# Performance work log

Hardware: AMD Instinct MI355X
Metric: run time of the kernel (lower is better)

The kernel has to match this reference:

```python
import jax, jax.numpy as jnp
import numpy as np

N_WIRES = 8


def setup_inputs() -> dict:
    key = jax.random.key(0)
    k1, k2, k3 = jax.random.split(key, 3)
    B, S, E = 8, 1024, 64
    x = jax.random.normal(k1, (B, S, E), jnp.float32)
    theta = jax.random.normal(k2, (N_WIRES,), jnp.float32) * 0.1  # trainable RX angles (shared QLayer across heads)
    V_CAT = 16
    combine_w = jax.random.normal(k3, (E, V_CAT), jnp.float32) / jnp.sqrt(jnp.float32(V_CAT))
    combine_b = jnp.zeros((E,), jnp.float32)
    return {"x": x, "theta": theta, "combine_w": combine_w, "combine_b": combine_b}


def _cnot(state, c, t):
    # state: [N] + [2]*N_WIRES ; wire w lives on axis w+1
    ca, ta = c + 1, t + 1
    s0 = jax.lax.index_in_dim(state, 0, axis=ca, keepdims=False)
    s1 = jax.lax.index_in_dim(state, 1, axis=ca, keepdims=False)
    ta2 = ta - 1 if ta > ca else ta  # control axis was removed
    s1 = jnp.flip(s1, axis=ta2)      # flip target bit where control == 1
    return jnp.stack([s0, s1], axis=ca)


def _qlayer(angles, theta):
    # angles: [N, 8]. RX(x) then trainable RX(theta) on same wire == RX(x+theta).
    half = 0.5 * (angles + theta)
    amp0 = jnp.cos(half).astype(jnp.complex64)          # <0|RX|0>
    amp1 = (-1j) * jnp.sin(half).astype(jnp.complex64)  # <1|RX|0>
    N = angles.shape[0]
    # product state over 8 wires -> [N, 256]
    state = jnp.ones((N, 1), jnp.complex64)
    for w in range(N_WIRES):
        per = jnp.stack([amp0[:, w], amp1[:, w]], axis=-1)  # [N, 2]
        state = (state[:, :, None] * per[:, None, :]).reshape(N, -1)
    state = state.reshape((N,) + (2,) * N_WIRES)
    # CNOT chain 0->1, ..., 6->7, then ring closure 7->0
    for w in range(N_WIRES - 1):
        state = _cnot(state, w, w + 1)
    state = _cnot(state, N_WIRES - 1, 0)
    probs = state.real ** 2 + state.imag ** 2
    exps = []
    for w in range(N_WIRES):
        axes = tuple(ax for ax in range(1, N_WIRES + 1) if ax != w + 1)
        marg = probs.sum(axis=axes)  # [N, 2]
        exps.append(marg[:, 0] - marg[:, 1])  # <Z_w>
    return jnp.stack(exps, axis=-1)  # [N, 8]


def reference(x, theta, combine_w, combine_b):
    B, S, E = x.shape
    d_k = E // N_WIRES  # == 8 (encoder needs exactly 8 angles)
    heads = x.reshape(B, S, N_WIRES, d_k).transpose(0, 2, 1, 3)  # [B, H, S, 8]
    meas = _qlayer(heads.reshape(-1, d_k), theta).reshape(B, N_WIRES, S, N_WIRES)
    # torch.chunk(3, -1) on size 8 -> splits of 3, 3, 2
    q, k, v = meas[..., :3], meas[..., 3:6], meas[..., 6:]
    scores = jnp.einsum('bhsd,bhtd->bhst', q, k) / jnp.sqrt(jnp.float32(E))
    attn = jax.nn.softmax(scores, axis=-1)
    out = jnp.einsum('bhst,bhtd->bhsd', attn, v)          # [B, H, S, 2]
    out = out.transpose(0, 2, 1, 3).reshape(B, S, -1)     # [B, S, 16]
    return out @ combine_w.T + combine_b
```

## Files before the change

kernel.cpp:

```cpp
#include <hip/hip_runtime.h>
#include <hip/hip_fp16.h>

#define NB 8
#define NS 1024
#define NH 8

typedef float f2 __attribute__((ext_vector_type(2)));

#if __has_builtin(__builtin_amdgcn_exp2f)
#define EXP2F(x) __builtin_amdgcn_exp2f(x)
#else
#define EXP2F(x) exp2f(x)
#endif


__global__ __launch_bounds__(256, 2) void attn_fused(
        const float* __restrict__ x, const float* __restrict__ theta,
        float* __restrict__ att) {
    __shared__ float4 kvl[NS];
    __shared__ __align__(16) float v1l[NS];
    __shared__ float redS[8][130];
    __shared__ float redA[8][130];
    __shared__ float redB[8][130];

    const int tid = threadIdx.x;
    const int bh = blockIdx.x >> 3;
    const int chunk = blockIdx.x & 7;
    const int b = bh >> 3, h = bh & 7;
    const int s0 = chunk * 128;

    float th[8];
#pragma unroll
    for (int j = 0; j < 8; ++j) th[j] = theta[j];

#pragma unroll
    for (int i = 0; i < 4; ++i) {
        int t = tid + i * 256;
        const float4* xp = (const float4*)(x + (((size_t)(b * NS + t)) << 6) + h * 8);
        float4 lo = xp[0], hi = xp[1];
        float c0 = __cosf(lo.x + th[0]);
        float c1 = __cosf(lo.y + th[1]);
        float c2 = __cosf(lo.z + th[2]);
        float c3 = __cosf(lo.w + th[3]);
        float c4 = __cosf(hi.x + th[4]);
        float c5 = __cosf(hi.y + th[5]);
        float c6 = __cosf(hi.z + th[6]);
        float c7 = __cosf(hi.w + th[7]);
        float m3 = ((c0 * c1) * c2) * c3;
        float m4 = m3 * c4;
        float m5 = m4 * c5;
        float m6 = m5 * c6;
        kvl[t] = make_float4(m3, m4, m5, m6);
        v1l[t] = m6 * c7;
    }

    const float QSC = 0.125f * 1.44269504088896f;
    const int sIdx = tid & 31;
    const int slice = tid >> 5;
    f2 qx[2], qy[2], qz[2];
#pragma unroll
    for (int p = 0; p < 2; ++p)
#pragma unroll
        for (int i = 0; i < 2; ++i) {
            int s = s0 + sIdx + (p * 2 + i) * 32;
            const float4* xp = (const float4*)(x + (((size_t)(b * NS + s)) << 6) + h * 8);
            float4 lo = xp[0], hi = xp[1];
            float c0 = __cosf(lo.x + th[0]);
            float c1 = __cosf(lo.y + th[1]);
            float c2 = __cosf(lo.z + th[2]);
            float c3 = __cosf(lo.w + th[3]);
            float c4 = __cosf(hi.x + th[4]);
            float c5 = __cosf(hi.y + th[5]);
            float c6 = __cosf(hi.z + th[6]);
            float c7 = __cosf(hi.w + th[7]);
            float m1 = c0 * c1;
            float m2 = m1 * c2;
            float m0 = ((c1 * c2) * (c3 * c4)) * ((c5 * c6) * c7);
            qx[p][i] = m0 * QSC;
            qy[p][i] = m1 * QSC;
            qz[p][i] = m2 * QSC;
        }
    __syncthreads();

    f2 sum[2] = {{0.f, 0.f}, {0.f, 0.f}};
    f2 A0[2]  = {{0.f, 0.f}, {0.f, 0.f}};
    f2 A1[2]  = {{0.f, 0.f}, {0.f, 0.f}};
    const int t0 = slice * 128;
    const float4* v1g4 = (const float4*)v1l;
#pragma unroll 2
    for (int g = 0; g < 32; ++g) {
        float4 v14 = v1g4[(t0 >> 2) + g];
        float4 kv0 = kvl[t0 + g * 4 + 0];
        float4 kv1 = kvl[t0 + g * 4 + 1];
        float4 kv2 = kvl[t0 + g * 4 + 2];
        float4 kv3 = kvl[t0 + g * 4 + 3];
        const float vv[4] = {v14.x, v14.y, v14.z, v14.w};
        const float4 kvs[4] = {kv0, kv1, kv2, kv3};
#pragma unroll
        for (int j = 0; j < 4; ++j) {
            float4 kv = kvs[j];
            float v1 = vv[j];
#pragma unroll
            for (int p = 0; p < 2; ++p) {
                f2 d = qx[p] * kv.x;
                d += qy[p] * kv.y;
                d += qz[p] * kv.z;
                f2 e = {EXP2F(d.x), EXP2F(d.y)};
                sum[p] += e;
                A0[p] += e * kv.w;
                A1[p] += e * v1;
            }
        }
    }

    redS[slice][sIdx]      = sum[0].x;
    redS[slice][sIdx + 32] = sum[0].y;
    redS[slice][sIdx + 64] = sum[1].x;
    redS[slice][sIdx + 96] = sum[1].y;
    redA[slice][sIdx]      = A0[0].x;
    redA[slice][sIdx + 32] = A0[0].y;
    redA[slice][sIdx + 64] = A0[1].x;
    redA[slice][sIdx + 96] = A0[1].y;
    redB[slice][sIdx]      = A1[0].x;
    redB[slice][sIdx + 32] = A1[0].y;
    redB[slice][sIdx + 64] = A1[1].x;
    redB[slice][sIdx + 96] = A1[1].y;
    __syncthreads();

    if (tid < 128) {
        float S = 0.f, A = 0.f, B = 0.f;
#pragma unroll
        for (int k = 0; k < 8; ++k) {
            S += redS[k][tid];
            A += redA[k][tid];
            B += redB[k][tid];
        }
        float inv = 1.0f / S;
        int s = s0 + tid;
        float* o = att + ((size_t)(b * NS + s) * 16) + h * 2;
        o[0] = A * inv;
        o[1] = B * inv;
    }
}

__global__ __launch_bounds__(256, 2) void proj_kernel(
        const float* __restrict__ att, const float* __restrict__ W,
        const float* __restrict__ bias, float* __restrict__ out) {
    __shared__ float WtL[16 * 65];
    __shared__ float biasL[64];
    __shared__ float rowsL[16 * 16];
    const int tid = threadIdx.x;
    const int rbase = blockIdx.x * 16;

    for (int i = tid; i < 1024; i += 256)
        WtL[(i & 15) * 65 + (i >> 4)] = W[i];
    if (tid < 64) biasL[tid] = bias[tid];
    if (tid < 256) rowsL[tid] = att[(size_t)rbase * 16 + tid];
    __syncthreads();

    const int e = tid & 63, rr = tid >> 6;
#pragma unroll
    for (int p = 0; p < 4; ++p) {
        int row = p * 4 + rr;
        float acc = biasL[e];
#pragma unroll
        for (int j = 0; j < 16; ++j)
            acc = fmaf(rowsL[row * 16 + j], WtL[j * 65 + e], acc);
        out[(((size_t)(rbase + row)) << 6) + e] = acc;
    }
}

#define NPAD 1028
#define SPB 32
__global__ __launch_bounds__(256) void fused_kernel(const float* __restrict__ x,
                                                    const float* __restrict__ theta,
                                                    const float* __restrict__ W,
                                                    const float* __restrict__ bias,
                                                    float* __restrict__ out) {
    __shared__ __half2 kvA[NH][NPAD];
    __shared__ __half2 kvB[NH][NPAD];
    __shared__ __half  kvC[NH][NPAD];
    __shared__ float   attl[SPB][17];
    __shared__ float   Wt[16][64];
    __shared__ float   bl[64];

    const int tid = threadIdx.x;
    const int b = blockIdx.x >> 5;
    const int chunk = blockIdx.x & 31;

    float th[8];
#pragma unroll
    for (int j = 0; j < 8; ++j) th[j] = theta[j];

    for (int i = tid; i < 1024; i += 256) Wt[i & 15][i >> 4] = W[i];
    if (tid < 64) bl[tid] = bias[tid];

    for (int i = 0; i < 32; ++i) {
        int r = tid + (i << 8);
        int h = r & 7, t = r >> 3;
        const float4* xp = (const float4*)(x + (((size_t)(b * NS + t)) << 6) + h * 8);
        float4 lo = xp[0], hi = xp[1];
        float c0 = __cosf(lo.x + th[0]);
        float c1 = __cosf(lo.y + th[1]);
        float c2 = __cosf(lo.z + th[2]);
        float c3 = __cosf(lo.w + th[3]);
        float c4 = __cosf(hi.x + th[4]);
        float c5 = __cosf(hi.y + th[5]);
        float c6 = __cosf(hi.z + th[6]);
        float c7 = __cosf(hi.w + th[7]);
        float m3 = ((c0 * c1) * c2) * c3;
        float m4 = m3 * c4;
        float m5 = m4 * c5;
        float m6 = m5 * c6;
        float m7 = m6 * c7;
        kvA[h][t] = __floats2half2_rn(m3, m4);
        kvB[h][t] = __floats2half2_rn(m5, m6);
        kvC[h][t] = __float2half_rn(m7);
    }
    __syncthreads();

    {
        const int h = tid >> 5;
        const int sl = tid & 31;
        const int sg = chunk * SPB + sl;
        const float4* xp = (const float4*)(x + (((size_t)(b * NS + sg)) << 6) + h * 8);
        float4 lo = xp[0], hi = xp[1];
        float c0 = __cosf(lo.x + th[0]);
        float c1 = __cosf(lo.y + th[1]);
        float c2 = __cosf(lo.z + th[2]);
        float c3 = __cosf(lo.w + th[3]);
        float c4 = __cosf(hi.x + th[4]);
        float c5 = __cosf(hi.y + th[5]);
        float c6 = __cosf(hi.z + th[6]);
        float c7 = __cosf(hi.w + th[7]);
        float m1 = c0 * c1;
        float m2 = m1 * c2;
        float m0 = ((c1 * c2) * (c3 * c4)) * ((c5 * c6) * c7);
        float q0 = m0 * 0.125f, q1 = m1 * 0.125f, q2 = m2 * 0.125f;

        float sum = 0.f, a0 = 0.f, a1 = 0.f;
#pragma unroll 4
        for (int t = 0; t < NS; ++t) {
            float2 kk = __half22float2(kvA[h][t]);
            float2 kv = __half22float2(kvB[h][t]);
            float v1 = __half2float(kvC[h][t]);
            float sc = q0 * kk.x + q1 * kk.y + q2 * kv.x;
            float e = __expf(sc);
            sum += e;
            a0 += e * kv.y;
            a1 += e * v1;
        }
        float inv = 1.0f / sum;
        attl[sl][h * 2] = a0 * inv;
        attl[sl][h * 2 + 1] = a1 * inv;
    }
    __syncthreads();

    {
        const int e = tid & 63;
        const int rr = tid >> 6;
#pragma unroll
        for (int i = 0; i < 8; ++i) {
            int sl = rr * 8 + i;
            float acc = bl[e];
#pragma unroll
            for (int j = 0; j < 16; ++j)
                acc += attl[sl][j] * Wt[j][e];
            int sg = chunk * SPB + sl;
            out[(((size_t)(b * NS + sg)) << 6) + e] = acc;
        }
    }
}

extern "C" void kernel_launch(void* const* d_in, const int* in_sizes, int n_in,
                              void* d_out, int out_size, void* d_ws, size_t ws_size,
                              hipStream_t stream) {
    const float* x     = (const float*)d_in[0];
    const float* theta = (const float*)d_in[1];
    const float* W     = (const float*)d_in[2];
    const float* bias  = (const float*)d_in[3];
    float* out = (float*)d_out;

    if (ws_size >= (size_t)NB * NS * 16 * sizeof(float)) {
        float* att = (float*)d_ws;
        attn_fused<<<dim3(NB * NH * 8), dim3(256), 0, stream>>>(x, theta, att);
        proj_kernel<<<dim3(NB * NS / 16), dim3(256), 0, stream>>>(att, W, bias, out);
    } else {
        fused_kernel<<<dim3(NB * (NS / SPB)), dim3(256), 0, stream>>>(x, theta, W, bias, out);
    }
}
```

Measured before the change: 78.45 us.

## Halve query chunk per block, double grid, reduce partials with wave shuffles

Each attention block now handles 64 queries instead of 128. The grid doubles to 1024 blocks, 16 slices each cover 64 keys, and occupancy is raised to 4 blocks per SM. The cross-slice reduction first sums partials inside each wave with xor shuffles and then combines the four waves through a small shared buffer. This exposes more parallelism and makes the reduction cheaper. The cost is that every block still recomputes all 1024 key/value features, so redundant x reads and cosine work double.

```diff
diff --git a/kernel.cpp b/kernel.cpp
--- a/kernel.cpp
+++ b/kernel.cpp
@@ -14,20 +14,20 @@
 #endif
 
 
-__global__ __launch_bounds__(256, 2) void attn_fused(
+__global__ __launch_bounds__(256, 4) void attn_fused(
         const float* __restrict__ x, const float* __restrict__ theta,
         float* __restrict__ att) {
     __shared__ float4 kvl[NS];
     __shared__ __align__(16) float v1l[NS];
-    __shared__ float redS[8][130];
-    __shared__ float redA[8][130];
-    __shared__ float redB[8][130];
+    __shared__ float redS[4][68];
+    __shared__ float redA[4][68];
+    __shared__ float redB[4][68];
 
     const int tid = threadIdx.x;
-    const int bh = blockIdx.x >> 3;
-    const int chunk = blockIdx.x & 7;
+    const int bh = blockIdx.x >> 4;
+    const int chunk = blockIdx.x & 15;
     const int b = bh >> 3, h = bh & 7;
-    const int s0 = chunk * 128;
+    const int s0 = chunk * 64;
 
     float th[8];
 #pragma unroll
@@ -55,14 +55,14 @@
     }
 
     const float QSC = 0.125f * 1.44269504088896f;
-    const int sIdx = tid & 31;
-    const int slice = tid >> 5;
+    const int sIdx = tid & 15;
+    const int slice = tid >> 4;
     f2 qx[2], qy[2], qz[2];
 #pragma unroll
     for (int p = 0; p < 2; ++p)
 #pragma unroll
         for (int i = 0; i < 2; ++i) {
-            int s = s0 + sIdx + (p * 2 + i) * 32;
+            int s = s0 + sIdx + (p * 2 + i) * 16;
             const float4* xp = (const float4*)(x + (((size_t)(b * NS + s)) << 6) + h * 8);
             float4 lo = xp[0], hi = xp[1];
             float c0 = __cosf(lo.x + th[0]);
@@ -85,10 +85,10 @@
     f2 sum[2] = {{0.f, 0.f}, {0.f, 0.f}};
     f2 A0[2]  = {{0.f, 0.f}, {0.f, 0.f}};
     f2 A1[2]  = {{0.f, 0.f}, {0.f, 0.f}};
-    const int t0 = slice * 128;
+    const int t0 = slice * 64;
     const float4* v1g4 = (const float4*)v1l;
-#pragma unroll 2
-    for (int g = 0; g < 32; ++g) {
+#pragma unroll 4
+    for (int g = 0; g < 16; ++g) {
         float4 v14 = v1g4[(t0 >> 2) + g];
         float4 kv0 = kvl[t0 + g * 4 + 0];
         float4 kv1 = kvl[t0 + g * 4 + 1];
@@ -113,28 +113,36 @@
         }
     }
 
-    redS[slice][sIdx]      = sum[0].x;
-    redS[slice][sIdx + 32] = sum[0].y;
-    redS[slice][sIdx + 64] = sum[1].x;
-    redS[slice][sIdx + 96] = sum[1].y;
-    redA[slice][sIdx]      = A0[0].x;
-    redA[slice][sIdx + 32] = A0[0].y;
-    redA[slice][sIdx + 64] = A0[1].x;
-    redA[slice][sIdx + 96] = A0[1].y;
-    redB[slice][sIdx]      = A1[0].x;
-    redB[slice][sIdx + 32] = A1[0].y;
-    redB[slice][sIdx + 64] = A1[1].x;
-    redB[slice][sIdx + 96] = A1[1].y;
-    __syncthreads();
-
-    if (tid < 128) {
-        float S = 0.f, A = 0.f, B = 0.f;
-#pragma unroll
-        for (int k = 0; k < 8; ++k) {
-            S += redS[k][tid];
-            A += redA[k][tid];
-            B += redB[k][tid];
-        }
+#pragma unroll
+    for (int m = 16; m <= 32; m <<= 1) {
+#pragma unroll
+        for (int p = 0; p < 2; ++p) {
+            sum[p].x += __shfl_xor(sum[p].x, m, 64);
+            sum[p].y += __shfl_xor(sum[p].y, m, 64);
+            A0[p].x  += __shfl_xor(A0[p].x, m, 64);
+            A0[p].y  += __shfl_xor(A0[p].y, m, 64);
+            A1[p].x  += __shfl_xor(A1[p].x, m, 64);
+            A1[p].y  += __shfl_xor(A1[p].y, m, 64);
+        }
+    }
+    const int w = tid >> 6;
+    if ((tid & 63) < 16) {
+#pragma unroll
+        for (int p = 0; p < 2; ++p)
+#pragma unroll
+            for (int i = 0; i < 2; ++i) {
+                int sl = sIdx + (p * 2 + i) * 16;
+                redS[w][sl] = (i == 0) ? sum[p].x : sum[p].y;
+                redA[w][sl] = (i == 0) ? A0[p].x : A0[p].y;
+                redB[w][sl] = (i == 0) ? A1[p].x : A1[p].y;
+            }
+    }
+    __syncthreads();
+
+    if (tid < 64) {
+        float S = redS[0][tid] + redS[1][tid] + redS[2][tid] + redS[3][tid];
+        float A = redA[0][tid] + redA[1][tid] + redA[2][tid] + redA[3][tid];
+        float B = redB[0][tid] + redB[1][tid] + redB[2][tid] + redB[3][tid];
         float inv = 1.0f / S;
         int s = s0 + tid;
         float* o = att + ((size_t)(b * NS + s) * 16) + h * 2;
@@ -283,7 +291,7 @@
 
     if (ws_size >= (size_t)NB * NS * 16 * sizeof(float)) {
         float* att = (float*)d_ws;
-        attn_fused<<<dim3(NB * NH * 8), dim3(256), 0, stream>>>(x, theta, att);
+        attn_fused<<<dim3(NB * NH * 16), dim3(256), 0, stream>>>(x, theta, att);
         proj_kernel<<<dim3(NB * NS / 16), dim3(256), 0, stream>>>(att, W, bias, out);
     } else {
         fused_kernel<<<dim3(NB * (NS / SPB)), dim3(256), 0, stream>>>(x, theta, W, bias, out);
```

After: 80.34 us. 1.02x slower.
